# Performance work log

Measured on AMD Instinct MI355X. Metric: run time of the kernel, lower is better.

The kernel has to match this reference:

```python
import jax, jax.numpy as jnp
import numpy as np

D = 768
H = 12
MLP = 3072
EPS = 1e-5


def _layernorm(x, g, b):
    mu = jnp.mean(x, axis=-1, keepdims=True)
    var = jnp.var(x, axis=-1, keepdims=True)
    return (x - mu) * jax.lax.rsqrt(var + EPS) * g + b


def setup_inputs() -> dict:
    key = jax.random.key(0)
    ks = jax.random.split(key, 16)
    s = 0.02
    inp = {
        "x": jax.random.normal(ks[0], (8, 1024, D), dtype=jnp.float32),
        "ln1_g": jnp.ones((D,), jnp.float32),
        "ln1_b": jnp.zeros((D,), jnp.float32),
        "Wq": jax.random.normal(ks[1], (D, D), jnp.float32) * s,
        "bq": jnp.zeros((D,), jnp.float32),
        "Wk": jax.random.normal(ks[2], (D, D), jnp.float32) * s,
        "bk": jnp.zeros((D,), jnp.float32),
        "Wv": jax.random.normal(ks[3], (D, D), jnp.float32) * s,
        "bv": jnp.zeros((D,), jnp.float32),
        "Wo": jax.random.normal(ks[4], (D, D), jnp.float32) * s,
        "bo": jnp.zeros((D,), jnp.float32),
        "ln2_g": jnp.ones((D,), jnp.float32),
        "ln2_b": jnp.zeros((D,), jnp.float32),
        "W1": jax.random.normal(ks[5], (D, MLP), jnp.float32) * s,
        "b1": jnp.zeros((MLP,), jnp.float32),
        "W2": jax.random.normal(ks[6], (MLP, D), jnp.float32) * s,
        "b2": jnp.zeros((D,), jnp.float32),
    }
    return inp


def reference(x, ln1_g, ln1_b, Wq, bq, Wk, bk, Wv, bv, Wo, bo, ln2_g, ln2_b, W1, b1, W2, b2):
    b, n, d = x.shape
    dh = d // H
    scale = 1.0 / jnp.sqrt(jnp.float32(d))  # NOTE: sqrt(input_dim), per source

    h = _layernorm(x, ln1_g, ln1_b)
    q = (h @ Wq + bq).reshape(b, n, H, dh).transpose(0, 2, 1, 3)  # bhnf
    k = (h @ Wk + bk).reshape(b, n, H, dh).transpose(0, 2, 1, 3)
    v = (h @ Wv + bv).reshape(b, n, H, dh).transpose(0, 2, 1, 3)

    score = jax.nn.softmax(jnp.einsum('bhif,bhjf->bhij', q, k) * scale, axis=-1)
    attn = jnp.einsum('bhij,bhjf->bihf', score, v).reshape(b, n, d)
    out = attn @ Wo + bo + x  # residual (dropout p=0)

    h2 = _layernorm(out, ln2_g, ln2_b)
    mlp = jax.nn.gelu(jax.nn.gelu(h2 @ W1 + b1, approximate=False) @ W2 + b2, approximate=False)
    return mlp + out
```

## Files before the change

### kernel.cpp

```cpp
#include <hip/hip_runtime.h>
#include <hip/hip_bf16.h>
#include <math.h>

typedef __bf16 bf16x8 __attribute__((ext_vector_type(8)));
typedef float f32x4 __attribute__((ext_vector_type(4)));

#define DD 768
#define HH 12
#define MLPD 3072
#define QSCALE 0.036084391824351615f

__device__ __forceinline__ float gelu_fast(float x) {
    float y = 1.5957691216057308f * x + 0.07135481283154893f * x * x * x;
    return x * __builtin_amdgcn_rcpf(1.0f + __expf(-y));
}

__device__ __forceinline__ void gload16(const void* g, void* l) {
    __builtin_amdgcn_global_load_lds(
        (const __attribute__((address_space(1))) unsigned int*)g,
        (__attribute__((address_space(3))) unsigned int*)l, 16, 0, 0);
}

__device__ __forceinline__ void ln_row(const float* __restrict__ xr,
                                       const float* __restrict__ g,
                                       const float* __restrict__ b,
                                       __bf16* __restrict__ orow, int lane) {
    float4 v[3];
    float s = 0.f, ss = 0.f;
#pragma unroll
    for (int i = 0; i < 3; ++i) {
        v[i] = *reinterpret_cast<const float4*>(&xr[(i * 64 + lane) * 4]);
        s += v[i].x + v[i].y + v[i].z + v[i].w;
        ss += v[i].x * v[i].x + v[i].y * v[i].y + v[i].z * v[i].z + v[i].w * v[i].w;
    }
#pragma unroll
    for (int m = 1; m < 64; m <<= 1) {
        s += __shfl_xor(s, m);
        ss += __shfl_xor(ss, m);
    }
    float mu = s * (1.0f / DD);
    float rstd = rsqrtf(ss * (1.0f / DD) - mu * mu + 1e-5f);
#pragma unroll
    for (int i = 0; i < 3; ++i) {
        int c = (i * 64 + lane) * 4;
        float4 gv = *reinterpret_cast<const float4*>(&g[c]);
        float4 bv = *reinterpret_cast<const float4*>(&b[c]);
        union { __bf16 h[4]; uint2 u; } o;
        o.h[0] = (__bf16)((v[i].x - mu) * rstd * gv.x + bv.x);
        o.h[1] = (__bf16)((v[i].y - mu) * rstd * gv.y + bv.y);
        o.h[2] = (__bf16)((v[i].z - mu) * rstd * gv.z + bv.z);
        o.h[3] = (__bf16)((v[i].w - mu) * rstd * gv.w + bv.w);
        *reinterpret_cast<uint2*>(&orow[c]) = o.u;
    }
}

__global__ __launch_bounds__(256) void ln_kernel(const float* __restrict__ X,
                                                 const float* __restrict__ g,
                                                 const float* __restrict__ b,
                                                 __bf16* __restrict__ O) {
    int row = blockIdx.x * 4 + (threadIdx.x >> 6);
    ln_row(X + (size_t)row * DD, g, b, O + (size_t)row * DD, threadIdx.x & 63);
}

__global__ __launch_bounds__(256) void prep_kernel(
    const float* __restrict__ Wq, const float* __restrict__ Wk,
    const float* __restrict__ Wv, const float* __restrict__ Wo,
    const float* __restrict__ W1, const float* __restrict__ W2,
    __bf16* __restrict__ wqkv, __bf16* __restrict__ wo,
    __bf16* __restrict__ w1, __bf16* __restrict__ w2,
    const float* __restrict__ x, const float* __restrict__ ln1_g,
    const float* __restrict__ ln1_b, __bf16* __restrict__ h) {
    __shared__ float tile[64][65];
    int blk = blockIdx.x;
    if (blk >= 1728) {
        int row = (blk - 1728) * 4 + (threadIdx.x >> 6);
        ln_row(x + (size_t)row * DD, ln1_g, ln1_b, h + (size_t)row * DD, threadIdx.x & 63);
        return;
    }
    const float* W; __bf16* Wt; int K, N, tk, tn;
    if (blk < 432) {
        int wsel = blk / 144, r = blk - wsel * 144;
        W = wsel == 0 ? Wq : (wsel == 1 ? Wk : Wv);
        Wt = wqkv + (size_t)wsel * 768 * 768;
        K = 768; N = 768; tk = r % 12; tn = r / 12;
    } else if (blk < 576) {
        int r = blk - 432; W = Wo; Wt = wo; K = 768; N = 768; tk = r % 12; tn = r / 12;
    } else if (blk < 1152) {
        int r = blk - 576; W = W1; Wt = w1; K = 768; N = 3072; tk = r % 12; tn = r / 12;
    } else {
        int r = blk - 1152; W = W2; Wt = w2; K = 3072; N = 768; tk = r % 48; tn = r / 48;
    }
    int k0 = tk * 64, n0 = tn * 64;
    int t = threadIdx.x;
    int tr = t >> 6, tc = t & 63;
#pragma unroll
    for (int i = 0; i < 16; ++i) {
        int row = i * 4 + tr;
        tile[row][tc] = W[(size_t)(k0 + row) * N + n0 + tc];
    }
    __syncthreads();
#pragma unroll
    for (int i = 0; i < 16; ++i) {
        int row = i * 4 + tr;
        Wt[(size_t)(n0 + row) * K + k0 + tc] = (__bf16)tile[tc][row];
    }
}

template <int EPI>
__global__ __launch_bounds__(512, 4) void gemm_pl(
    const __bf16* __restrict__ A, const __bf16* __restrict__ Bt,
    const float* __restrict__ b0, const float* __restrict__ b1, const float* __restrict__ b2,
    void* __restrict__ o0, void* __restrict__ o1, void* __restrict__ o2,
    const float* __restrict__ resid, int M, int N, int K) {
    extern __shared__ __bf16 lds[];
    __bf16* As = lds;
    __bf16* Bs = lds + 16384;
    const int t = threadIdx.x;
    const int w = t >> 6, lane = t & 63;
    const int wm = w >> 2, wn = w & 3;
    const int lr = lane & 15, lg = lane >> 4;
    const int m0 = blockIdx.x * 128, n0 = blockIdx.y * 128;
    const int lrow8 = lane >> 3;
    const int cSwz = ((lane & 7) ^ lrow8) * 8;

    const __bf16* aSrc = A + (size_t)(m0 + w * 16 + lrow8) * K + cSwz;
    const __bf16* bSrc = Bt + (size_t)(n0 + w * 16 + lrow8) * K + cSwz;
    const int ldsW = w * 16 * 64;

    const int nt = K >> 6;
    f32x4 acc[4][2] = {};

    auto stage = [&](int T) {
        const int buf = (T & 1) * 8192;
#pragma unroll
        for (int c = 0; c < 2; ++c)
            gload16(aSrc + (size_t)(c * 8) * K + T * 64, &As[buf + ldsW + c * 8 * 64]);
#pragma unroll
        for (int c = 0; c < 2; ++c)
            gload16(bSrc + (size_t)(c * 8) * K + T * 64, &Bs[buf + ldsW + c * 8 * 64]);
    };

    stage(0);
    for (int T = 0; T < nt; ++T) {
        if (T + 1 < nt) {
            stage(T + 1);
            asm volatile("s_waitcnt vmcnt(4)" ::: "memory");
        } else {
            asm volatile("s_waitcnt vmcnt(0)" ::: "memory");
        }
        __builtin_amdgcn_s_barrier();
        const int buf = (T & 1) * 8192;
#pragma unroll
        for (int kg = 0; kg < 2; ++kg) {
            bf16x8 af[4], bfr[2];
#pragma unroll
            for (int i = 0; i < 4; ++i)
                af[i] = *reinterpret_cast<const bf16x8*>(
                    &As[buf + (wm * 64 + i * 16 + lr) * 64 + (((kg << 2) | lg) ^ (lr & 7)) * 8]);
#pragma unroll
            for (int j = 0; j < 2; ++j)
                bfr[j] = *reinterpret_cast<const bf16x8*>(
                    &Bs[buf + (wn * 32 + j * 16 + lr) * 64 + (((kg << 2) | lg) ^ (lr & 7)) * 8]);
#pragma unroll
            for (int i = 0; i < 4; ++i)
#pragma unroll
                for (int j = 0; j < 2; ++j)
                    acc[i][j] = __builtin_amdgcn_mfma_f32_16x16x32_bf16(bfr[j], af[i], acc[i][j], 0, 0, 0);
        }
        __builtin_amdgcn_s_barrier();
    }

#pragma unroll
    for (int i = 0; i < 4; ++i) {
        const int m = m0 + wm * 64 + i * 16 + lr;
        const int bI = m >> 10, ntok = m & 1023;
#pragma unroll
        for (int j = 0; j < 2; ++j) {
            const int n = n0 + wn * 32 + j * 16 + lg * 4;
            if (EPI == 0) {
                const int wid = n / 768;
                const int cc0 = n - wid * 768;
                const int hh = cc0 >> 6, f0 = cc0 & 63;
                const float* bsel = (wid == 0 ? b0 : (wid == 1 ? b1 : b2));
                const float4 bv = *reinterpret_cast<const float4*>(&bsel[cc0]);
                const float v0 = acc[i][j][0] + bv.x, v1 = acc[i][j][1] + bv.y;
                const float v2 = acc[i][j][2] + bv.z, v3 = acc[i][j][3] + bv.w;
                if (wid == 0) {
                    union { __bf16 h[4]; uint2 u; } pk;
                    pk.h[0] = (__bf16)(v0 * QSCALE); pk.h[1] = (__bf16)(v1 * QSCALE);
                    pk.h[2] = (__bf16)(v2 * QSCALE); pk.h[3] = (__bf16)(v3 * QSCALE);
                    *reinterpret_cast<uint2*>(
                        &((__bf16*)o0)[((((size_t)(bI * HH + hh) << 10) + ntok) << 6) + f0]) = pk.u;
                } else if (wid == 1) {
                    union { __bf16 h[4]; uint2 u; } pk;
                    pk.h[0] = (__bf16)v0; pk.h[1] = (__bf16)v1;
                    pk.h[2] = (__bf16)v2; pk.h[3] = (__bf16)v3;
                    *reinterpret_cast<uint2*>(
                        &((__bf16*)o1)[((((size_t)(bI * HH + hh) << 10) + ntok) << 6) + f0]) = pk.u;
                } else {
                    __bf16* vb = (__bf16*)o2;
                    size_t base = ((size_t)(bI * HH + hh) * 64 + f0) << 10;
                    vb[base + ntok] = (__bf16)v0;
                    vb[base + (1 << 10) + ntok] = (__bf16)v1;
                    vb[base + (2 << 10) + ntok] = (__bf16)v2;
                    vb[base + (3 << 10) + ntok] = (__bf16)v3;
                }
            } else if (EPI == 3) {
                const float4 bv = *reinterpret_cast<const float4*>(&b0[n]);
                union { __bf16 h[4]; uint2 u; } pk;
                pk.h[0] = (__bf16)gelu_fast(acc[i][j][0] + bv.x);
                pk.h[1] = (__bf16)gelu_fast(acc[i][j][1] + bv.y);
                pk.h[2] = (__bf16)gelu_fast(acc[i][j][2] + bv.z);
                pk.h[3] = (__bf16)gelu_fast(acc[i][j][3] + bv.w);
                *reinterpret_cast<uint2*>(&((__bf16*)o0)[(size_t)m * MLPD + n]) = pk.u;
            } else {
                const float4 bv = *reinterpret_cast<const float4*>(&b0[n]);
                const float v0 = acc[i][j][0] + bv.x, v1 = acc[i][j][1] + bv.y;
                const float v2 = acc[i][j][2] + bv.z, v3 = acc[i][j][3] + bv.w;
                const float4 rv = *reinterpret_cast<const float4*>(&resid[(size_t)m * DD + n]);
                if (EPI == 2) {
                    float4 ov = {v0 + rv.x, v1 + rv.y, v2 + rv.z, v3 + rv.w};
                    *reinterpret_cast<float4*>(&((float*)o0)[(size_t)m * DD + n]) = ov;
                } else {
                    float4 ov = {gelu_fast(v0) + rv.x, gelu_fast(v1) + rv.y,
                                 gelu_fast(v2) + rv.z, gelu_fast(v3) + rv.w};
                    *reinterpret_cast<float4*>(&((float*)o0)[(size_t)m * DD + n]) = ov;
                }
            }
        }
    }
}

__global__ __launch_bounds__(512, 6) void attn_kernel(
    const __bf16* __restrict__ Q, const __bf16* __restrict__ Kg,
    const __bf16* __restrict__ Vt, __bf16* __restrict__ Aout) {
    __shared__ char KsB[2][64 * 128];
    __shared__ char VsB[2][64 * 128];
    __shared__ char PsB[8][16 * 128];
    const int id = blockIdx.x;
    const int swz = (id & 7) * 96 + (id >> 3);
    const int bh = swz >> 3, qt = swz & 7;
    const int t = threadIdx.x, w = t >> 6, lane = t & 63;
    const int lr = lane & 15, lg = lane >> 4;
    const size_t bhN = (size_t)bh << 10;
    const int q0 = qt * 128;

    bf16x8 qf[2];
#pragma unroll
    for (int kg = 0; kg < 2; ++kg)
        qf[kg] = *reinterpret_cast<const bf16x8*>(&Q[(bhN + q0 + w * 16 + lr) * 64 + kg * 32 + lg * 8]);

    const int srow = t >> 3;
    const int sc = ((t & 7) ^ (srow & 7)) * 16;
    const char* kbase = (const char*)Kg + bhN * 128;
    const char* vbase = (const char*)Vt + ((size_t)bh << 17);
    const int wlds = w * 1024;

    f32x4 oacc[4] = {};
    float lsum[4] = {0.f, 0.f, 0.f, 0.f};

    gload16(kbase + (size_t)srow * 128 + sc, KsB[0] + wlds);
    gload16(vbase + (size_t)srow * 2048 + sc, VsB[0] + wlds);

    for (int kt = 0; kt < 16; ++kt) {
        const int buf = kt & 1;
        if (kt < 15) {
            gload16(kbase + (size_t)((kt + 1) * 64 + srow) * 128 + sc, KsB[buf ^ 1] + wlds);
            gload16(vbase + (size_t)srow * 2048 + (kt + 1) * 128 + sc, VsB[buf ^ 1] + wlds);
            asm volatile("s_waitcnt vmcnt(2)" ::: "memory");
        } else {
            asm volatile("s_waitcnt vmcnt(0)" ::: "memory");
        }
        __builtin_amdgcn_s_barrier();

        f32x4 s[4] = {};
        __builtin_amdgcn_s_setprio(1);
#pragma unroll
        for (int kg = 0; kg < 2; ++kg) {
#pragma unroll
            for (int j = 0; j < 4; ++j) {
                int row = j * 16 + lr;
                bf16x8 kf = *reinterpret_cast<const bf16x8*>(
                    KsB[buf] + ((row * 128 + kg * 64 + lg * 16) ^ ((row & 7) << 4)));
                s[j] = __builtin_amdgcn_mfma_f32_16x16x32_bf16(qf[kg], kf, s[j], 0, 0, 0);
            }
        }
        __builtin_amdgcn_s_setprio(0);

#pragma unroll
        for (int r = 0; r < 4; ++r) {
            int prow = lg * 4 + r;
#pragma unroll
            for (int j = 0; j < 2; ++j) {
                float pv = __expf(s[j][r]);
                lsum[r] += pv;
                *reinterpret_cast<__bf16*>(
                    PsB[w] + ((prow * 128 + (j * 16 + lr) * 2) ^ ((prow & 7) << 4))) = (__bf16)pv;
            }
        }
        bf16x8 pf0 = *reinterpret_cast<const bf16x8*>(
            PsB[w] + ((lr * 128 + 0 * 64 + lg * 16) ^ ((lr & 7) << 4)));
#pragma unroll
        for (int r = 0; r < 4; ++r) {
            int prow = lg * 4 + r;
#pragma unroll
            for (int j = 2; j < 4; ++j) {
                float pv = __expf(s[j][r]);
                lsum[r] += pv;
                *reinterpret_cast<__bf16*>(
                    PsB[w] + ((prow * 128 + (j * 16 + lr) * 2) ^ ((prow & 7) << 4))) = (__bf16)pv;
            }
        }
#pragma unroll
        for (int j = 0; j < 4; ++j) {
            int row = j * 16 + lr;
            bf16x8 vf = *reinterpret_cast<const bf16x8*>(
                VsB[buf] + ((row * 128 + 0 * 64 + lg * 16) ^ ((row & 7) << 4)));
            oacc[j] = __builtin_amdgcn_mfma_f32_16x16x32_bf16(pf0, vf, oacc[j], 0, 0, 0);
        }
        bf16x8 pf1 = *reinterpret_cast<const bf16x8*>(
            PsB[w] + ((lr * 128 + 1 * 64 + lg * 16) ^ ((lr & 7) << 4)));
#pragma unroll
        for (int j = 0; j < 4; ++j) {
            int row = j * 16 + lr;
            bf16x8 vf = *reinterpret_cast<const bf16x8*>(
                VsB[buf] + ((row * 128 + 1 * 64 + lg * 16) ^ ((row & 7) << 4)));
            oacc[j] = __builtin_amdgcn_mfma_f32_16x16x32_bf16(pf1, vf, oacc[j], 0, 0, 0);
        }
        __builtin_amdgcn_s_barrier();
    }

#pragma unroll
    for (int r = 0; r < 4; ++r)
#pragma unroll
        for (int m = 1; m < 16; m <<= 1) lsum[r] += __shfl_xor(lsum[r], m);

    const int bI = bh / HH, hh = bh % HH;
#pragma unroll
    for (int r = 0; r < 4; ++r) {
        float inv = 1.0f / lsum[r];
        int qrow = q0 + w * 16 + lg * 4 + r;
        size_t base = ((size_t)(bI << 10) + qrow) * DD + hh * 64;
#pragma unroll
        for (int j = 0; j < 4; ++j)
            Aout[base + j * 16 + lr] = (__bf16)(oacc[j][r] * inv);
    }
}

extern "C" void kernel_launch(void* const* d_in, const int* in_sizes, int n_in,
                              void* d_out, int out_size, void* d_ws, size_t ws_size,
                              hipStream_t stream) {
    const float* x     = (const float*)d_in[0];
    const float* ln1_g = (const float*)d_in[1];
    const float* ln1_b = (const float*)d_in[2];
    const float* Wq    = (const float*)d_in[3];
    const float* bq    = (const float*)d_in[4];
    const float* Wk    = (const float*)d_in[5];
    const float* bk    = (const float*)d_in[6];
    const float* Wv    = (const float*)d_in[7];
    const float* bv    = (const float*)d_in[8];
    const float* Wo    = (const float*)d_in[9];
    const float* bo    = (const float*)d_in[10];
    const float* ln2_g = (const float*)d_in[11];
    const float* ln2_b = (const float*)d_in[12];
    const float* W1    = (const float*)d_in[13];
    const float* b1    = (const float*)d_in[14];
    const float* W2    = (const float*)d_in[15];
    const float* b2    = (const float*)d_in[16];

    char* p = (char*)d_ws;
    auto alloc = [&](size_t bytes) { char* r = p; p += bytes; return r; };
    __bf16* wqkv_t = (__bf16*)alloc((size_t)2304 * 768 * 2);
    __bf16* wo_t   = (__bf16*)alloc((size_t)768 * 768 * 2);
    __bf16* w1_t   = (__bf16*)alloc((size_t)3072 * 768 * 2);
    __bf16* w2_t   = (__bf16*)alloc((size_t)768 * 3072 * 2);
    __bf16* h      = (__bf16*)alloc((size_t)8192 * 768 * 2);
    float*  outb   = (float*) alloc((size_t)8192 * 768 * 4);
    __bf16* q      = (__bf16*)alloc((size_t)8192 * 768 * 2);
    __bf16* kb     = (__bf16*)alloc((size_t)8192 * 768 * 2);
    __bf16* vt     = (__bf16*)alloc((size_t)8192 * 768 * 2);
    __bf16* attn   = (__bf16*)alloc((size_t)8192 * 768 * 2);
    __bf16* mid    = q;

    const int LDSP = 65536;
    hipFuncSetAttribute(reinterpret_cast<const void*>(gemm_pl<0>),
                        hipFuncAttributeMaxDynamicSharedMemorySize, LDSP);
    hipFuncSetAttribute(reinterpret_cast<const void*>(gemm_pl<2>),
                        hipFuncAttributeMaxDynamicSharedMemorySize, LDSP);
    hipFuncSetAttribute(reinterpret_cast<const void*>(gemm_pl<3>),
                        hipFuncAttributeMaxDynamicSharedMemorySize, LDSP);
    hipFuncSetAttribute(reinterpret_cast<const void*>(gemm_pl<4>),
                        hipFuncAttributeMaxDynamicSharedMemorySize, LDSP);

    prep_kernel<<<3776, 256, 0, stream>>>(Wq, Wk, Wv, Wo, W1, W2,
                                          wqkv_t, wo_t, w1_t, w2_t,
                                          x, ln1_g, ln1_b, h);
    gemm_pl<0><<<dim3(64, 18), 512, LDSP, stream>>>(h, wqkv_t, bq, bk, bv, q, kb, vt,
                                                    nullptr, 8192, 2304, 768);
    attn_kernel<<<768, 512, 0, stream>>>(q, kb, vt, attn);
    gemm_pl<2><<<dim3(64, 6), 512, LDSP, stream>>>(attn, wo_t, bo, nullptr, nullptr, outb,
                                                   nullptr, nullptr, x, 8192, 768, 768);
    ln_kernel<<<2048, 256, 0, stream>>>(outb, ln2_g, ln2_b, h);
    gemm_pl<3><<<dim3(64, 24), 512, LDSP, stream>>>(h, w1_t, b1, nullptr, nullptr, mid,
                                                    nullptr, nullptr, nullptr, 8192, 3072, 768);
    gemm_pl<4><<<dim3(64, 6), 512, LDSP, stream>>>(mid, w2_t, b2, nullptr, nullptr, (float*)d_out,
                                                   nullptr, nullptr, outb, 8192, 768, 3072);
}
```

Measured before the change: 226.8 us.

## Shrink GEMM block tile to 64x128 with 4 waves for more blocks

Reworks the pipelined GEMM so each 256-thread block computes a 64x128 tile instead of 128x128 with 512 threads. Each wave now covers all 64 rows and its own 32-column slice. Global-to-LDS staging becomes 6 unified 16-byte loads per lane that cover both the A and B tiles, and the LDS footprint drops. This doubles the grid size for better CU fill and load balance. In exchange, each block reuses the B tile across fewer rows, which adds global and L2 traffic.

```diff
diff --git a/kernel.cpp b/kernel.cpp
--- a/kernel.cpp
+++ b/kernel.cpp
@@ -107,60 +107,68 @@
 }
 
 template <int EPI>
-__global__ __launch_bounds__(512, 4) void gemm_pl(
+__global__ __launch_bounds__(256, 3) void gemm_pl(
     const __bf16* __restrict__ A, const __bf16* __restrict__ Bt,
     const float* __restrict__ b0, const float* __restrict__ b1, const float* __restrict__ b2,
     void* __restrict__ o0, void* __restrict__ o1, void* __restrict__ o2,
     const float* __restrict__ resid, int M, int N, int K) {
     extern __shared__ __bf16 lds[];
-    __bf16* As = lds;
-    __bf16* Bs = lds + 16384;
     const int t = threadIdx.x;
     const int w = t >> 6, lane = t & 63;
-    const int wm = w >> 2, wn = w & 3;
     const int lr = lane & 15, lg = lane >> 4;
-    const int m0 = blockIdx.x * 128, n0 = blockIdx.y * 128;
+    const int m0 = blockIdx.x * 64, n0 = blockIdx.y * 128;
     const int lrow8 = lane >> 3;
     const int cSwz = ((lane & 7) ^ lrow8) * 8;
 
-    const __bf16* aSrc = A + (size_t)(m0 + w * 16 + lrow8) * K + cSwz;
-    const __bf16* bSrc = Bt + (size_t)(n0 + w * 16 + lrow8) * K + cSwz;
-    const int ldsW = w * 16 * 64;
+    const __bf16* usrc[6];
+    int ulds[6], utog[6];
+#pragma unroll
+    for (int c = 0; c < 6; ++c) {
+        int u = w * 6 + c;
+        if (u < 8) {
+            int row = u * 8 + lrow8;
+            usrc[c] = A + (size_t)(m0 + row) * K + cSwz;
+            ulds[c] = u * 512;
+            utog[c] = 4096;
+        } else {
+            int row = (u - 8) * 8 + lrow8;
+            usrc[c] = Bt + (size_t)(n0 + row) * K + cSwz;
+            ulds[c] = 8192 + (u - 8) * 512;
+            utog[c] = 8192;
+        }
+    }
 
     const int nt = K >> 6;
     f32x4 acc[4][2] = {};
 
     auto stage = [&](int T) {
-        const int buf = (T & 1) * 8192;
-#pragma unroll
-        for (int c = 0; c < 2; ++c)
-            gload16(aSrc + (size_t)(c * 8) * K + T * 64, &As[buf + ldsW + c * 8 * 64]);
-#pragma unroll
-        for (int c = 0; c < 2; ++c)
-            gload16(bSrc + (size_t)(c * 8) * K + T * 64, &Bs[buf + ldsW + c * 8 * 64]);
+        const int tb = (T & 1);
+#pragma unroll
+        for (int c = 0; c < 6; ++c)
+            gload16(usrc[c] + (size_t)T * 64, &lds[ulds[c] + tb * utog[c]]);
     };
 
     stage(0);
     for (int T = 0; T < nt; ++T) {
         if (T + 1 < nt) {
             stage(T + 1);
-            asm volatile("s_waitcnt vmcnt(4)" ::: "memory");
+            asm volatile("s_waitcnt vmcnt(6)" ::: "memory");
         } else {
             asm volatile("s_waitcnt vmcnt(0)" ::: "memory");
         }
         __builtin_amdgcn_s_barrier();
-        const int buf = (T & 1) * 8192;
+        const int bufA = (T & 1) * 4096, bufB = 8192 + (T & 1) * 8192;
 #pragma unroll
         for (int kg = 0; kg < 2; ++kg) {
             bf16x8 af[4], bfr[2];
 #pragma unroll
             for (int i = 0; i < 4; ++i)
                 af[i] = *reinterpret_cast<const bf16x8*>(
-                    &As[buf + (wm * 64 + i * 16 + lr) * 64 + (((kg << 2) | lg) ^ (lr & 7)) * 8]);
+                    &lds[bufA + (i * 16 + lr) * 64 + (((kg << 2) | lg) ^ (lr & 7)) * 8]);
 #pragma unroll
             for (int j = 0; j < 2; ++j)
                 bfr[j] = *reinterpret_cast<const bf16x8*>(
-                    &Bs[buf + (wn * 32 + j * 16 + lr) * 64 + (((kg << 2) | lg) ^ (lr & 7)) * 8]);
+                    &lds[bufB + (w * 32 + j * 16 + lr) * 64 + (((kg << 2) | lg) ^ (lr & 7)) * 8]);
 #pragma unroll
             for (int i = 0; i < 4; ++i)
 #pragma unroll
@@ -172,11 +180,11 @@
 
 #pragma unroll
     for (int i = 0; i < 4; ++i) {
-        const int m = m0 + wm * 64 + i * 16 + lr;
+        const int m = m0 + i * 16 + lr;
         const int bI = m >> 10, ntok = m & 1023;
 #pragma unroll
         for (int j = 0; j < 2; ++j) {
-            const int n = n0 + wn * 32 + j * 16 + lg * 4;
+            const int n = n0 + w * 32 + j * 16 + lg * 4;
             if (EPI == 0) {
                 const int wid = n / 768;
                 const int cc0 = n - wid * 768;
@@ -382,7 +390,7 @@
     __bf16* attn   = (__bf16*)alloc((size_t)8192 * 768 * 2);
     __bf16* mid    = q;
 
-    const int LDSP = 65536;
+    const int LDSP = 49152;
     hipFuncSetAttribute(reinterpret_cast<const void*>(gemm_pl<0>),
                         hipFuncAttributeMaxDynamicSharedMemorySize, LDSP);
     hipFuncSetAttribute(reinterpret_cast<const void*>(gemm_pl<2>),
@@ -395,14 +403,14 @@
     prep_kernel<<<3776, 256, 0, stream>>>(Wq, Wk, Wv, Wo, W1, W2,
                                           wqkv_t, wo_t, w1_t, w2_t,
                                           x, ln1_g, ln1_b, h);
-    gemm_pl<0><<<dim3(64, 18), 512, LDSP, stream>>>(h, wqkv_t, bq, bk, bv, q, kb, vt,
-                                                    nullptr, 8192, 2304, 768);
+    gemm_pl<0><<<dim3(128, 18), 256, LDSP, stream>>>(h, wqkv_t, bq, bk, bv, q, kb, vt,
+                                                     nullptr, 8192, 2304, 768);
     attn_kernel<<<768, 512, 0, stream>>>(q, kb, vt, attn);
-    gemm_pl<2><<<dim3(64, 6), 512, LDSP, stream>>>(attn, wo_t, bo, nullptr, nullptr, outb,
-                                                   nullptr, nullptr, x, 8192, 768, 768);
+    gemm_pl<2><<<dim3(128, 6), 256, LDSP, stream>>>(attn, wo_t, bo, nullptr, nullptr, outb,
+                                                    nullptr, nullptr, x, 8192, 768, 768);
     ln_kernel<<<2048, 256, 0, stream>>>(outb, ln2_g, ln2_b, h);
-    gemm_pl<3><<<dim3(64, 24), 512, LDSP, stream>>>(h, w1_t, b1, nullptr, nullptr, mid,
-                                                    nullptr, nullptr, nullptr, 8192, 3072, 768);
-    gemm_pl<4><<<dim3(64, 6), 512, LDSP, stream>>>(mid, w2_t, b2, nullptr, nullptr, (float*)d_out,
-                                                   nullptr, nullptr, outb, 8192, 768, 3072);
-}
+    gemm_pl<3><<<dim3(128, 24), 256, LDSP, stream>>>(h, w1_t, b1, nullptr, nullptr, mid,
+                                                     nullptr, nullptr, nullptr, 8192, 3072, 768);
+    gemm_pl<4><<<dim3(128, 6), 256, LDSP, stream>>>(mid, w2_t, b2, nullptr, nullptr, (float*)d_out,
+                                                    nullptr, nullptr, outb, 8192, 768, 3072);
+}
```

Result: slower. 237.5 us (+4.8%).
